# Kernel optimization log

Hardware: AMD Instinct MI355X
Metric: run time of the kernel (lower is better)

Reference implementation:

```python
import jax, jax.numpy as jnp
import numpy as np

D_MODEL = 1024
NUM_HEADS = 16
D_K = D_MODEL // NUM_HEADS


def setup_inputs() -> dict:
    key = jax.random.key(0)
    ks = jax.random.split(key, 9)
    B, S = 4, 2048
    s = 1.0 / np.sqrt(D_MODEL)
    return {
        "x": jax.random.normal(ks[0], (B, S, D_MODEL), dtype=jnp.float32),
        "Wq": jax.random.uniform(ks[1], (D_MODEL, D_MODEL), jnp.float32, -s, s),
        "bq": jax.random.uniform(ks[2], (D_MODEL,), jnp.float32, -s, s),
        "Wk": jax.random.uniform(ks[3], (D_MODEL, D_MODEL), jnp.float32, -s, s),
        "bk": jax.random.uniform(ks[4], (D_MODEL,), jnp.float32, -s, s),
        "Wv": jax.random.uniform(ks[5], (D_MODEL, D_MODEL), jnp.float32, -s, s),
        "bv": jax.random.uniform(ks[6], (D_MODEL,), jnp.float32, -s, s),
        "Wo": jax.random.uniform(ks[7], (D_MODEL, D_MODEL), jnp.float32, -s, s),
        "bo": jax.random.uniform(ks[8], (D_MODEL,), jnp.float32, -s, s),
    }


def reference(x, Wq, bq, Wk, bk, Wv, bv, Wo, bo):
    B, S, D = x.shape
    H, dk = NUM_HEADS, D_K

    def proj(W, b):
        # [B,S,D] -> [B,H,S,dk]  (torch Linear: x @ W^T + b)
        y = jnp.einsum('bsd,ed->bse', x, W) + b
        return y.reshape(B, S, H, dk).transpose(0, 2, 1, 3)

    Q = proj(Wq, bq)
    K = proj(Wk, bk)
    V = proj(Wv, bv)

    scale = 1.0 / jnp.sqrt(jnp.asarray(dk, x.dtype))
    scores = jnp.einsum('bhqd,bhkd->bhqk', Q, K) * scale  # [B,H,S,S]
    attn = jax.nn.softmax(scores, axis=-1)
    # dropout is identity in eval mode
    out = jnp.einsum('bhqk,bhkd->bhqd', attn, V)  # [B,H,S,dk]
    out = out.transpose(0, 2, 1, 3).reshape(B, S, D)
    return jnp.einsum('bsd,ed->bse', out, Wo) + bo
```

## Files before the change

### kernel.cpp

```cpp
#include <hip/hip_runtime.h>


typedef unsigned short u16;
typedef unsigned int u32;
typedef __attribute__((ext_vector_type(8))) short bf16x8;
typedef __attribute__((ext_vector_type(4))) float f32x4;
typedef __attribute__((ext_vector_type(4))) unsigned short u16x4;
typedef __attribute__((ext_vector_type(8))) unsigned short u16x8;

#define SEQ    2048
#define DMODEL 1024
#define NHEAD  16
#define DK     64
#define BATCH  4
#define MROWS  (BATCH * SEQ)
#define LCF    0.18033688011112042f

__device__ __forceinline__ u16 f2bf(float f) {
  unsigned int u = __float_as_uint(f);
  u += 0x7fffu + ((u >> 16) & 1u);
  return (u16)(u >> 16);
}

__device__ __forceinline__ void gload_lds16(const void* g, void* l) {
  __builtin_amdgcn_global_load_lds((const __attribute__((address_space(1))) void*)g,
                                   (__attribute__((address_space(3))) void*)l,
                                   16, 0, 0);
}

__global__ __launch_bounds__(256) void cvt_all(const float* __restrict__ x,
                                               const float* __restrict__ w0,
                                               const float* __restrict__ w1,
                                               const float* __restrict__ w2,
                                               const float* __restrict__ w3,
                                               u16* xb, u16* o0, u16* o1, u16* o2, u16* o3) {
  const int NX4 = MROWS * DMODEL / 4;
  int i = blockIdx.x * 256 + threadIdx.x;
  const float* src; u16* dst; int off;
  if (i < NX4) { src = x; dst = xb; off = i; }
  else {
    int j = i - NX4;
    int wi = j >> 18; off = j & 0x3FFFF;
    src = wi == 0 ? w0 : wi == 1 ? w1 : wi == 2 ? w2 : w3;
    dst = wi == 0 ? o0 : wi == 1 ? o1 : wi == 2 ? o2 : o3;
  }
  float4 v = ((const float4*)src)[off];
  u16x4 o;
  o.x = f2bf(v.x); o.y = f2bf(v.y); o.z = f2bf(v.z); o.w = f2bf(v.w);
  ((u16x4*)dst)[off] = o;
}

template <int OUT_F32>
__device__ __forceinline__ void gemm_body(const u16* __restrict__ A,
                                          const u16* __restrict__ Bw,
                                          const float* __restrict__ bias,
                                          void* __restrict__ outp,
                                          int bm, int bn, int M, int N, int K,
                                          float scale, int vt_mode,
                                          u16* As, u16* Bs) {
  const int t = threadIdx.x, w = t >> 6, l = t & 63;
  const int wr = (w >> 1) * 64, wc = (w & 1) * 64;
  const int lrow = l & 15, kgrp = l >> 4;
  const int r_in = l >> 3;
  const int c_in = ((l & 7) ^ r_in) * 8;
  const int sw = lrow & 7;

  f32x4 acc[4][4] = {};

  for (int kt = 0; kt < K; kt += 64) {
#pragma unroll
    for (int it = 0; it < 4; ++it) {
      const int chunk = w * 4 + it;
      const int row = chunk * 8 + r_in;
      gload_lds16(A  + (size_t)(bm * 128 + row) * K + kt + c_in, (char*)As + chunk * 1024);
      gload_lds16(Bw + (size_t)(bn * 128 + row) * K + kt + c_in, (char*)Bs + chunk * 1024);
    }
    __syncthreads();
#pragma unroll
    for (int kc = 0; kc < 2; ++kc) {
      bf16x8 af[4], bfr[4];
      const int slot = (kc * 4 + kgrp) ^ sw;
#pragma unroll
      for (int m = 0; m < 4; ++m)
        af[m] = *(const bf16x8*)&As[(wr + m * 16 + lrow) * 64 + slot * 8];
#pragma unroll
      for (int n = 0; n < 4; ++n)
        bfr[n] = *(const bf16x8*)&Bs[(wc + n * 16 + lrow) * 64 + slot * 8];
#pragma unroll
      for (int m = 0; m < 4; ++m)
#pragma unroll
        for (int n = 0; n < 4; ++n)
          acc[m][n] = __builtin_amdgcn_mfma_f32_16x16x32_bf16(af[m], bfr[n], acc[m][n], 0, 0, 0);
    }
    __syncthreads();
  }

  const int cr0 = bm * 128 + wr, cc0 = bn * 128 + wc;
  if (!OUT_F32 && vt_mode) {
    const int s0 = (bm & 15) * 128 + wr + kgrp * 4;
    u16* vtp = (u16*)outp + (size_t)(bm >> 4) * 1024 * 2048;
#pragma unroll
    for (int n = 0; n < 4; ++n) {
      const int col = cc0 + n * 16 + lrow;
      const float bv = bias[col];
#pragma unroll
      for (int m = 0; m < 4; ++m) {
        u16x4 pk;
#pragma unroll
        for (int r = 0; r < 4; ++r) pk[r] = f2bf(acc[m][n][r] + bv);
        *(u16x4*)&vtp[(size_t)col * 2048 + s0 + m * 16] = pk;
      }
    }
    return;
  }
#pragma unroll
  for (int n = 0; n < 4; ++n) {
    const int col = cc0 + n * 16 + lrow;
    const float bv = bias[col];
#pragma unroll
    for (int m = 0; m < 4; ++m) {
#pragma unroll
      for (int r = 0; r < 4; ++r) {
        const int row = cr0 + m * 16 + kgrp * 4 + r;
        const float v = (acc[m][n][r] + bv) * scale;
        if (OUT_F32) ((float*)outp)[(size_t)row * N + col] = v;
        else         ((u16*)outp)[(size_t)row * N + col] = f2bf(v);
      }
    }
  }
}

__global__ __launch_bounds__(256) void gemm_bt_f32(const u16* __restrict__ A,
                                                   const u16* __restrict__ Bw,
                                                   const float* __restrict__ bias,
                                                   float* __restrict__ outp) {
  __shared__ u16 As[128 * 64];
  __shared__ u16 Bs[128 * 64];
  const int wg = blockIdx.x;
  const int xcd = wg & 7, local = wg >> 3;
  const int lm = local & 7, bn = local >> 3;
  const int bm = xcd * 8 + lm;
  gemm_body<1>(A, Bw, bias, outp, bm, bn, MROWS, DMODEL, DMODEL, 1.0f, 0, As, Bs);
}

__global__ __launch_bounds__(256) void gemm_qkv(const u16* __restrict__ A,
                                                const u16* __restrict__ W0,
                                                const u16* __restrict__ W1,
                                                const u16* __restrict__ W2,
                                                const float* __restrict__ b0,
                                                const float* __restrict__ b1,
                                                const float* __restrict__ b2,
                                                u16* o0, u16* o1, u16* vt) {
  __shared__ u16 As[128 * 64];
  __shared__ u16 Bs[128 * 64];
  const int wg = blockIdx.x;
  const int xcd = wg & 7, local = wg >> 3;
  const int lm = local & 7, lnsel = local >> 3;
  const int bm = xcd * 8 + lm;
  const int sel = lnsel >> 3, bn = lnsel & 7;
  const u16* Bw = sel == 0 ? W0 : sel == 1 ? W1 : W2;
  const float* bias = sel == 0 ? b0 : sel == 1 ? b1 : b2;
  u16* outp = sel == 0 ? o0 : sel == 1 ? o1 : vt;
  const float scale = sel == 0 ? LCF : 1.0f;
  gemm_body<0>(A, Bw, bias, outp, bm, bn, MROWS, DMODEL, DMODEL, scale,
               sel == 2 ? 1 : 0, As, Bs);
}

__global__ __launch_bounds__(256, 4) void attn_kernel(const u16* __restrict__ Qg,
                                                      const u16* __restrict__ Kg,
                                                      const u16* __restrict__ Vt,
                                                      u16* __restrict__ Og) {
  __shared__ u16 Ks[2][64 * 64];
  __shared__ u16 Vs[3][64 * 64];

  const int t = threadIdx.x, w = t >> 6, l = t & 63;
  const int lrow = l & 15, kgrp = l >> 4;
  const int sw = lrow & 7;

  const int id = blockIdx.x;
  const int swzid = (id & 7) * 128 + (id >> 3);
  const int qt = swzid & 15, bh = swzid >> 4;
  const int b = bh >> 4, h = bh & 15;
  const size_t base  = (size_t)b * SEQ * DMODEL + h * DK;
  const size_t vbase = (size_t)bh * DK * SEQ;
  const int r_in = l >> 3;
  const int c_in = ((l & 7) ^ r_in) * 8;

  int kro[2];
#pragma unroll
  for (int it = 0; it < 2; ++it) {
    const int p = (w * 2 + it) * 8 + r_in;
    const int n_ = p >> 4, g_ = (p >> 2) & 3, rr = p & 3;
    kro[it] = (n_ >> 1) * 32 + g_ * 8 + (n_ & 1) * 4 + rr;
  }

  const int qr = qt * 128 + w * 32;
  bf16x8 aq[2][2];
#pragma unroll
  for (int rg = 0; rg < 2; ++rg) {
    const u16* qp = Qg + base + (size_t)(qr + rg * 16 + lrow) * DMODEL + kgrp * 8;
    aq[rg][0] = *(const bf16x8*)qp;
    aq[rg][1] = *(const bf16x8*)(qp + 32);
  }

  f32x4 o_acc[2][4] = {};
  f32x4 sc[2][4];
  bf16x8 paA[2][2], paB[2][2];
  float lsum[2] = {};

#define STAGE(kt_, kb_, vb_)                                                    \
  {                                                                             \
    const int k0_ = (kt_) * 64;                                                 \
    _Pragma("unroll")                                                           \
    for (int it = 0; it < 2; ++it) {                                            \
      const int chunk = w * 2 + it;                                             \
      const int r = chunk * 8 + r_in;                                           \
      gload_lds16(Kg + base + (size_t)(k0_ + kro[it]) * DMODEL + c_in,          \
                  (char*)&Ks[kb_][0] + chunk * 1024);                           \
      gload_lds16(Vt + vbase + (size_t)r * SEQ + k0_ + c_in,                    \
                  (char*)&Vs[vb_][0] + chunk * 1024);                           \
    }                                                                           \
  }

#define QK_BLOCK(KB)                                                            \
  {                                                                             \
    f32x4 z = {};                                                               \
    sc[0][0]=z; sc[0][1]=z; sc[0][2]=z; sc[0][3]=z;                             \
    sc[1][0]=z; sc[1][1]=z; sc[1][2]=z; sc[1][3]=z;                             \
    __builtin_amdgcn_s_setprio(1);                                              \
    _Pragma("unroll")                                                           \
    for (int kc = 0; kc < 2; ++kc) {                                            \
      const int slot = (kc * 4 + kgrp) ^ sw;                                    \
      _Pragma("unroll")                                                         \
      for (int n = 0; n < 4; ++n) {                                             \
        bf16x8 bk = *(const bf16x8*)&Ks[KB][(n * 16 + lrow) * 64 + slot * 8];   \
        sc[0][n] = __builtin_amdgcn_mfma_f32_16x16x32_bf16(bk, aq[0][kc], sc[0][n], 0, 0, 0); \
        sc[1][n] = __builtin_amdgcn_mfma_f32_16x16x32_bf16(bk, aq[1][kc], sc[1][n], 0, 0, 0); \
      }                                                                         \
    }                                                                           \
    __builtin_amdgcn_s_setprio(0);                                              \
  }

#define SM_BLOCK(PA)                                                            \
  _Pragma("unroll")                                                             \
  for (int rg = 0; rg < 2; ++rg) {                                              \
    u32 pk[4][2];                                                               \
    float lp = 0.0f;                                                            \
    _Pragma("unroll")                                                           \
    for (int n = 0; n < 4; ++n) {                                               \
      const float p0 = __builtin_amdgcn_exp2f(sc[rg][n][0]);                    \
      const float p1 = __builtin_amdgcn_exp2f(sc[rg][n][1]);                    \
      const float p2 = __builtin_amdgcn_exp2f(sc[rg][n][2]);                    \
      const float p3 = __builtin_amdgcn_exp2f(sc[rg][n][3]);                    \
      lp += (p0 + p1) + (p2 + p3);                                              \
      asm("v_cvt_pk_bf16_f32 %0, %1, %2" : "=v"(pk[n][0]) : "v"(p0), "v"(p1));  \
      asm("v_cvt_pk_bf16_f32 %0, %1, %2" : "=v"(pk[n][1]) : "v"(p2), "v"(p3));  \
    }                                                                           \
    lsum[rg] += lp;                                                             \
    union { u32 u[4]; bf16x8 v; } f0, f1;                                       \
    f0.u[0] = pk[0][0]; f0.u[1] = pk[0][1]; f0.u[2] = pk[1][0]; f0.u[3] = pk[1][1]; \
    f1.u[0] = pk[2][0]; f1.u[1] = pk[2][1]; f1.u[2] = pk[3][0]; f1.u[3] = pk[3][1]; \
    PA[rg][0] = f0.v;                                                           \
    PA[rg][1] = f1.v;                                                           \
  }

#define PV_BLOCK(PA, VB)                                                        \
  {                                                                             \
    __builtin_amdgcn_s_setprio(1);                                              \
    _Pragma("unroll")                                                           \
    for (int kc = 0; kc < 2; ++kc) {                                            \
      const int slot = (kc * 4 + kgrp) ^ sw;                                    \
      _Pragma("unroll")                                                         \
      for (int n = 0; n < 4; ++n) {                                             \
        bf16x8 bv = *(const bf16x8*)&Vs[VB][(n * 16 + lrow) * 64 + slot * 8];   \
        o_acc[0][n] = __builtin_amdgcn_mfma_f32_16x16x32_bf16(PA[0][kc], bv, o_acc[0][n], 0, 0, 0); \
        o_acc[1][n] = __builtin_amdgcn_mfma_f32_16x16x32_bf16(PA[1][kc], bv, o_acc[1][n], 0, 0, 0); \
      }                                                                         \
    }                                                                           \
    __builtin_amdgcn_s_setprio(0);                                              \
  }

  STAGE(0, 0, 0);
  __syncthreads();
  STAGE(1, 1, 1);
  QK_BLOCK(0);
  SM_BLOCK(paA);

  int vi_w = 2, vi_r = 0;
#pragma unroll 1
  for (int jj = 0; jj < 15; ++jj) {
    __syncthreads();
    STAGE(2 + 2 * jj, 0, vi_w);
    vi_w = (vi_w == 2) ? 0 : vi_w + 1;
    QK_BLOCK(1);
    PV_BLOCK(paA, vi_r);
    vi_r = (vi_r == 2) ? 0 : vi_r + 1;
    SM_BLOCK(paB);

    __syncthreads();
    STAGE(3 + 2 * jj, 1, vi_w);
    vi_w = (vi_w == 2) ? 0 : vi_w + 1;
    QK_BLOCK(0);
    PV_BLOCK(paB, vi_r);
    vi_r = (vi_r == 2) ? 0 : vi_r + 1;
    SM_BLOCK(paA);
  }
  __syncthreads();
  QK_BLOCK(1);
  PV_BLOCK(paA, vi_r);
  vi_r = (vi_r == 2) ? 0 : vi_r + 1;
  SM_BLOCK(paB);
  PV_BLOCK(paB, vi_r);

#undef STAGE
#undef QK_BLOCK
#undef SM_BLOCK
#undef PV_BLOCK

#pragma unroll
  for (int rg = 0; rg < 2; ++rg) {
    float Lq = lsum[rg];
    Lq += __shfl_xor(Lq, 16);
    Lq += __shfl_xor(Lq, 32);
#pragma unroll
    for (int r = 0; r < 4; ++r) {
      const float inv = 1.0f / __shfl(Lq, kgrp * 4 + r);
      const int row = qr + rg * 16 + kgrp * 4 + r;
#pragma unroll
      for (int n = 0; n < 4; ++n)
        Og[base + (size_t)row * DMODEL + n * 16 + lrow] = f2bf(o_acc[rg][n][r] * inv);
    }
  }
}

extern "C" void kernel_launch(void* const* d_in, const int* in_sizes, int n_in,
                              void* d_out, int out_size, void* d_ws, size_t ws_size,
                              hipStream_t stream) {
  const float* x  = (const float*)d_in[0];
  const float* Wq = (const float*)d_in[1];
  const float* bq = (const float*)d_in[2];
  const float* Wk = (const float*)d_in[3];
  const float* bk = (const float*)d_in[4];
  const float* Wv = (const float*)d_in[5];
  const float* bv = (const float*)d_in[6];
  const float* Wo = (const float*)d_in[7];
  const float* bo = (const float*)d_in[8];
  float* out = (float*)d_out;

  const size_t XB   = (size_t)MROWS * DMODEL * 2;
  const size_t WB   = (size_t)DMODEL * DMODEL * 2;
  const size_t NEED = XB * 5 + WB * 4;
  if (ws_size < NEED) return;

  char* ws = (char*)d_ws;
  u16* xb  = (u16*)(ws);
  u16* wqb = (u16*)(ws + XB);
  u16* wkb = (u16*)(ws + XB + WB);
  u16* wvb = (u16*)(ws + XB + 2 * WB);
  u16* wob = (u16*)(ws + XB + 3 * WB);
  u16* qb  = (u16*)(ws + XB + 4 * WB);
  u16* kb  = (u16*)(ws + 2 * XB + 4 * WB);
  u16* vt  = (u16*)(ws + 3 * XB + 4 * WB);
  u16* ab  = (u16*)(ws + 4 * XB + 4 * WB);

  const int NCVT = (MROWS * DMODEL / 4) + DMODEL * DMODEL;
  cvt_all<<<NCVT / 256, 256, 0, stream>>>(x, Wq, Wk, Wv, Wo, xb, wqb, wkb, wvb, wob);

  gemm_qkv<<<dim3(1536), 256, 0, stream>>>(xb, wqb, wkb, wvb,
                                           bq, bk, bv, qb, kb, vt);

  attn_kernel<<<dim3(1024), 256, 0, stream>>>(qb, kb, vt, ab);

  gemm_bt_f32<<<dim3(512), 256, 0, stream>>>(ab, wob, bo, out);
}
```

Before: 206.5 us.

## Double attention query tile per block to 256 rows and fuse QK with softmax

Result: faster. 175.7 us (-14.9%).

```diff
diff --git a/kernel.cpp b/kernel.cpp
--- a/kernel.cpp
+++ b/kernel.cpp
@@ -166,7 +166,7 @@
                sel == 2 ? 1 : 0, As, Bs);
 }
 
-__global__ __launch_bounds__(256, 4) void attn_kernel(const u16* __restrict__ Qg,
+__global__ __launch_bounds__(256, 2) void attn_kernel(const u16* __restrict__ Qg,
                                                       const u16* __restrict__ Kg,
                                                       const u16* __restrict__ Vt,
                                                       u16* __restrict__ Og) {
@@ -178,8 +178,8 @@
   const int sw = lrow & 7;
 
   const int id = blockIdx.x;
-  const int swzid = (id & 7) * 128 + (id >> 3);
-  const int qt = swzid & 15, bh = swzid >> 4;
+  const int swzid = (id & 7) * 64 + (id >> 3);
+  const int qt = swzid & 7, bh = swzid >> 3;
   const int b = bh >> 4, h = bh & 15;
   const size_t base  = (size_t)b * SEQ * DMODEL + h * DK;
   const size_t vbase = (size_t)bh * DK * SEQ;
@@ -194,19 +194,20 @@
     kro[it] = (n_ >> 1) * 32 + g_ * 8 + (n_ & 1) * 4 + rr;
   }
 
-  const int qr = qt * 128 + w * 32;
-  bf16x8 aq[2][2];
-#pragma unroll
-  for (int rg = 0; rg < 2; ++rg) {
+  const int qr = qt * 256 + w * 64;
+  bf16x8 aq[4][2];
+#pragma unroll
+  for (int rg = 0; rg < 4; ++rg) {
     const u16* qp = Qg + base + (size_t)(qr + rg * 16 + lrow) * DMODEL + kgrp * 8;
     aq[rg][0] = *(const bf16x8*)qp;
     aq[rg][1] = *(const bf16x8*)(qp + 32);
   }
 
-  f32x4 o_acc[2][4] = {};
-  f32x4 sc[2][4];
-  bf16x8 paA[2][2], paB[2][2];
-  float lsum[2] = {};
+  f32x4 o_acc[4][4] = {};
+  float lsum[4] = {};
+  bf16x8 paA[4][2], paB[4][2];
+  const int slot0 = (kgrp ^ sw) * 8;
+  const int slot1 = ((4 + kgrp) ^ sw) * 8;
 
 #define STAGE(kt_, kb_, vb_)                                                    \
   {                                                                             \
@@ -222,60 +223,63 @@
     }                                                                           \
   }
 
-#define QK_BLOCK(KB)                                                            \
+#define QKSM_BLOCK(KB, PA)                                                      \
   {                                                                             \
-    f32x4 z = {};                                                               \
-    sc[0][0]=z; sc[0][1]=z; sc[0][2]=z; sc[0][3]=z;                             \
-    sc[1][0]=z; sc[1][1]=z; sc[1][2]=z; sc[1][3]=z;                             \
-    __builtin_amdgcn_s_setprio(1);                                              \
-    _Pragma("unroll")                                                           \
-    for (int kc = 0; kc < 2; ++kc) {                                            \
-      const int slot = (kc * 4 + kgrp) ^ sw;                                    \
+    bf16x8 kf0[4], kf1[4];                                                      \
+    _Pragma("unroll")                                                           \
+    for (int n = 0; n < 4; ++n) {                                               \
+      kf0[n] = *(const bf16x8*)&Ks[KB][(n * 16 + lrow) * 64 + slot0];           \
+      kf1[n] = *(const bf16x8*)&Ks[KB][(n * 16 + lrow) * 64 + slot1];           \
+    }                                                                           \
+    _Pragma("unroll")                                                           \
+    for (int rg = 0; rg < 4; ++rg) {                                            \
+      f32x4 sc[4] = {};                                                         \
+      __builtin_amdgcn_s_setprio(1);                                            \
+      _Pragma("unroll")                                                         \
+      for (int n = 0; n < 4; ++n)                                               \
+        sc[n] = __builtin_amdgcn_mfma_f32_16x16x32_bf16(kf0[n], aq[rg][0], sc[n], 0, 0, 0); \
+      _Pragma("unroll")                                                         \
+      for (int n = 0; n < 4; ++n)                                               \
+        sc[n] = __builtin_amdgcn_mfma_f32_16x16x32_bf16(kf1[n], aq[rg][1], sc[n], 0, 0, 0); \
+      __builtin_amdgcn_s_setprio(0);                                            \
+      u32 pk[4][2];                                                             \
+      float lp = 0.0f;                                                          \
       _Pragma("unroll")                                                         \
       for (int n = 0; n < 4; ++n) {                                             \
-        bf16x8 bk = *(const bf16x8*)&Ks[KB][(n * 16 + lrow) * 64 + slot * 8];   \
-        sc[0][n] = __builtin_amdgcn_mfma_f32_16x16x32_bf16(bk, aq[0][kc], sc[0][n], 0, 0, 0); \
-        sc[1][n] = __builtin_amdgcn_mfma_f32_16x16x32_bf16(bk, aq[1][kc], sc[1][n], 0, 0, 0); \
+        const float p0 = __builtin_amdgcn_exp2f(sc[n][0]);                      \
+        const float p1 = __builtin_amdgcn_exp2f(sc[n][1]);                      \
+        const float p2 = __builtin_amdgcn_exp2f(sc[n][2]);                      \
+        const float p3 = __builtin_amdgcn_exp2f(sc[n][3]);                      \
+        lp += (p0 + p1) + (p2 + p3);                                            \
+        asm("v_cvt_pk_bf16_f32 %0, %1, %2" : "=v"(pk[n][0]) : "v"(p0), "v"(p1));\
+        asm("v_cvt_pk_bf16_f32 %0, %1, %2" : "=v"(pk[n][1]) : "v"(p2), "v"(p3));\
       }                                                                         \
-    }                                                                           \
-    __builtin_amdgcn_s_setprio(0);                                              \
-  }
-
-#define SM_BLOCK(PA)                                                            \
-  _Pragma("unroll")                                                             \
-  for (int rg = 0; rg < 2; ++rg) {                                              \
-    u32 pk[4][2];                                                               \
-    float lp = 0.0f;                                                            \
-    _Pragma("unroll")                                                           \
-    for (int n = 0; n < 4; ++n) {                                               \
-      const float p0 = __builtin_amdgcn_exp2f(sc[rg][n][0]);                    \
-      const float p1 = __builtin_amdgcn_exp2f(sc[rg][n][1]);                    \
-      const float p2 = __builtin_amdgcn_exp2f(sc[rg][n][2]);                    \
-      const float p3 = __builtin_amdgcn_exp2f(sc[rg][n][3]);                    \
-      lp += (p0 + p1) + (p2 + p3);                                              \
-      asm("v_cvt_pk_bf16_f32 %0, %1, %2" : "=v"(pk[n][0]) : "v"(p0), "v"(p1));  \
-      asm("v_cvt_pk_bf16_f32 %0, %1, %2" : "=v"(pk[n][1]) : "v"(p2), "v"(p3));  \
-    }                                                                           \
-    lsum[rg] += lp;                                                             \
-    union { u32 u[4]; bf16x8 v; } f0, f1;                                       \
-    f0.u[0] = pk[0][0]; f0.u[1] = pk[0][1]; f0.u[2] = pk[1][0]; f0.u[3] = pk[1][1]; \
-    f1.u[0] = pk[2][0]; f1.u[1] = pk[2][1]; f1.u[2] = pk[3][0]; f1.u[3] = pk[3][1]; \
-    PA[rg][0] = f0.v;                                                           \
-    PA[rg][1] = f1.v;                                                           \
+      lsum[rg] += lp;                                                           \
+      union { u32 u[4]; bf16x8 v; } f0, f1;                                     \
+      f0.u[0] = pk[0][0]; f0.u[1] = pk[0][1]; f0.u[2] = pk[1][0]; f0.u[3] = pk[1][1]; \
+      f1.u[0] = pk[2][0]; f1.u[1] = pk[2][1]; f1.u[2] = pk[3][0]; f1.u[3] = pk[3][1]; \
+      PA[rg][0] = f0.v;                                                         \
+      PA[rg][1] = f1.v;                                                         \
+    }                                                                           \
   }
 
 #define PV_BLOCK(PA, VB)                                                        \
   {                                                                             \
+    bf16x8 vf0[4], vf1[4];                                                      \
+    _Pragma("unroll")                                                           \
+    for (int n = 0; n < 4; ++n) {                                               \
+      vf0[n] = *(const bf16x8*)&Vs[VB][(n * 16 + lrow) * 64 + slot0];           \
+      vf1[n] = *(const bf16x8*)&Vs[VB][(n * 16 + lrow) * 64 + slot1];           \
+    }                                                                           \
     __builtin_amdgcn_s_setprio(1);                                              \
     _Pragma("unroll")                                                           \
-    for (int kc = 0; kc < 2; ++kc) {                                            \
-      const int slot = (kc * 4 + kgrp) ^ sw;                                    \
-      _Pragma("unroll")                                                         \
-      for (int n = 0; n < 4; ++n) {                                             \
-        bf16x8 bv = *(const bf16x8*)&Vs[VB][(n * 16 + lrow) * 64 + slot * 8];   \
-        o_acc[0][n] = __builtin_amdgcn_mfma_f32_16x16x32_bf16(PA[0][kc], bv, o_acc[0][n], 0, 0, 0); \
-        o_acc[1][n] = __builtin_amdgcn_mfma_f32_16x16x32_bf16(PA[1][kc], bv, o_acc[1][n], 0, 0, 0); \
-      }                                                                         \
+    for (int rg = 0; rg < 4; ++rg) {                                            \
+      _Pragma("unroll")                                                         \
+      for (int n = 0; n < 4; ++n)                                               \
+        o_acc[rg][n] = __builtin_amdgcn_mfma_f32_16x16x32_bf16(PA[rg][0], vf0[n], o_acc[rg][n], 0, 0, 0); \
+      _Pragma("unroll")                                                         \
+      for (int n = 0; n < 4; ++n)                                               \
+        o_acc[rg][n] = __builtin_amdgcn_mfma_f32_16x16x32_bf16(PA[rg][1], vf1[n], o_acc[rg][n], 0, 0, 0); \
     }                                                                           \
     __builtin_amdgcn_s_setprio(0);                                              \
   }
@@ -283,8 +287,7 @@
   STAGE(0, 0, 0);
   __syncthreads();
   STAGE(1, 1, 1);
-  QK_BLOCK(0);
-  SM_BLOCK(paA);
+  QKSM_BLOCK(0, paA);
 
   int vi_w = 2, vi_r = 0;
 #pragma unroll 1
@@ -292,33 +295,29 @@
     __syncthreads();
     STAGE(2 + 2 * jj, 0, vi_w);
     vi_w = (vi_w == 2) ? 0 : vi_w + 1;
-    QK_BLOCK(1);
+    QKSM_BLOCK(1, paB);
     PV_BLOCK(paA, vi_r);
     vi_r = (vi_r == 2) ? 0 : vi_r + 1;
-    SM_BLOCK(paB);
 
     __syncthreads();
     STAGE(3 + 2 * jj, 1, vi_w);
     vi_w = (vi_w == 2) ? 0 : vi_w + 1;
-    QK_BLOCK(0);
+    QKSM_BLOCK(0, paA);
     PV_BLOCK(paB, vi_r);
     vi_r = (vi_r == 2) ? 0 : vi_r + 1;
-    SM_BLOCK(paA);
   }
   __syncthreads();
-  QK_BLOCK(1);
+  QKSM_BLOCK(1, paB);
   PV_BLOCK(paA, vi_r);
   vi_r = (vi_r == 2) ? 0 : vi_r + 1;
-  SM_BLOCK(paB);
   PV_BLOCK(paB, vi_r);
 
 #undef STAGE
-#undef QK_BLOCK
-#undef SM_BLOCK
+#undef QKSM_BLOCK
 #undef PV_BLOCK
 
 #pragma unroll
-  for (int rg = 0; rg < 2; ++rg) {
+  for (int rg = 0; rg < 4; ++rg) {
     float Lq = lsum[rg];
     Lq += __shfl_xor(Lq, 16);
     Lq += __shfl_xor(Lq, 32);
@@ -369,7 +368,7 @@
   gemm_qkv<<<dim3(1536), 256, 0, stream>>>(xb, wqb, wkb, wvb,
                                            bq, bk, bv, qb, kb, vt);
 
-  attn_kernel<<<dim3(1024), 256, 0, stream>>>(qb, kb, vt, ab);
+  attn_kernel<<<dim3(512), 256, 0, stream>>>(qb, kb, vt, ab);
 
   gemm_bt_f32<<<dim3(512), 256, 0, stream>>>(ab, wob, bo, out);
 }
```
